# Performance work log

Measured on AMD Instinct MI355X. Metric: run time of the kernel, lower is better.

The kernel has to match this reference:

```python
import jax, jax.numpy as jnp
import numpy as np

HEADS = 8
LATENT_LEN = 64
SEQ_LEN = 8192
DIM = 512
DIM_HEAD = DIM // HEADS
LN_EPS = 1e-5


def setup_inputs() -> dict:
    key = jax.random.key(0)
    k1, k2, k3 = jax.random.split(key, 3)
    b, n = 16, SEQ_LEN + LATENT_LEN
    x = jax.random.normal(k1, (b, n, DIM), dtype=jnp.float32)
    # torch nn.Linear weights are [out_features, in_features]
    wq = jax.random.normal(k2, (DIM, DIM), dtype=jnp.float32) * (DIM ** -0.5)
    wkv = jax.random.normal(k3, (DIM, DIM), dtype=jnp.float32) * (DIM ** -0.5)
    ln_g = jnp.ones((DIM_HEAD,), dtype=jnp.float32)
    ln_b = jnp.zeros((DIM_HEAD,), dtype=jnp.float32)
    return {"x": x, "wq": wq, "wkv": wkv, "ln_g": ln_g, "ln_b": ln_b}


def _rotate_half(t):
    # lucidrains-style rotate_half: split last dim in two halves, (-x2, x1)
    d2 = t.shape[-1] // 2
    t1, t2 = t[..., :d2], t[..., d2:]
    return jnp.concatenate([-t2, t1], axis=-1)


def _rotary_emb(n, d, dtype):
    inv_freq = 1.0 / (10000.0 ** (jnp.arange(0, d, 2, dtype=jnp.float32) / d))
    freqs = jnp.arange(n, dtype=jnp.float32)[:, None] * inv_freq[None, :]  # [n, d/2]
    emb = jnp.concatenate([freqs, freqs], axis=-1)  # [n, d]
    return jnp.cos(emb).astype(dtype), jnp.sin(emb).astype(dtype)


def reference(x, wq, wkv, ln_g, ln_b):
    b, n, dim = x.shape
    h, d = HEADS, DIM_HEAD
    context_len = n - LATENT_LEN
    scale = d ** -0.5

    q = x @ wq.T   # [b, n, dim]
    kv = x @ wkv.T # [b, n, dim]
    # rearrange 'b n (h d) -> (b h) n d'
    to_bh = lambda t: t.reshape(b, n, h, d).transpose(0, 2, 1, 3).reshape(b * h, n, d)
    q, kv = to_bh(q), to_bh(kv)

    cos, sin = _rotary_emb(n, d, x.dtype)  # [n, d] broadcast over (b h)
    rope = lambda t: t * cos + _rotate_half(t) * sin
    q, kv = rope(q), rope(kv)

    q = q * scale
    q_latent = q[:, context_len:, :]  # [(b h), latent, d]

    # LayerNorm over head dim applied to V (kv)
    mu = jnp.mean(kv, axis=-1, keepdims=True)
    var = jnp.mean(jnp.square(kv - mu), axis=-1, keepdims=True)
    lkv = (kv - mu) * jax.lax.rsqrt(var + LN_EPS) * ln_g + ln_b

    sim = jnp.einsum('bid,bjd->bij', q_latent, kv)  # [(b h), latent, n]
    attn = jax.nn.softmax(sim, axis=-1)
    out = jnp.einsum('bij,bjd->bid', attn, lkv)     # [(b h), latent, d]

    # rearrange '(b h) n d -> b n (h d)'
    out = out.reshape(b, h, LATENT_LEN, d).transpose(0, 2, 1, 3).reshape(b, LATENT_LEN, dim)
    return out
```

## Files before the change

### kernel.cpp

```cpp
#include <hip/hip_runtime.h>
#include <hip/hip_bf16.h>
#include <math.h>

#define SEQ_LEN 8192
#define LAT 64
#define NPOS 8256
#define NBATCH 16
#define NHEADS 8
#define DH 64
#define DIM 512
#define NBH 128
#define NROWS 132096
#define NCHUNK 8
#define NTILES 129
#define TPC 17

typedef unsigned short u16;
typedef unsigned int   u32;
using short8 = __attribute__((ext_vector_type(8))) short;
using f32x4  = __attribute__((ext_vector_type(4))) float;

static __device__ __forceinline__ float bf2f(u16 u) {
  union { u32 i; float f; } v; v.i = ((u32)u) << 16; return v.f;
}
static __device__ __forceinline__ u16 f2bf(float f) {
  union { float f; u32 i; } v; v.f = f;
  u32 x = v.i;
  return (u16)((x + 0x7fffu + ((x >> 16) & 1u)) >> 16);
}
static __device__ __forceinline__ void gload_lds16(const void* g, void* l) {
  __builtin_amdgcn_global_load_lds(
      (const __attribute__((address_space(1))) unsigned int*)g,
      (__attribute__((address_space(3))) unsigned int*)l, 16, 0, 0);
}

__global__ void k_rtable(float* __restrict__ ctab, float* __restrict__ stab) {
  int idx = blockIdx.x * 256 + threadIdx.x;
  int pos = idx >> 5, i = idx & 31;
  float inv = (float)(1.0 / pow(10000.0, (double)(2 * i) / 64.0));
  float ang = (float)pos * inv;
  ctab[idx] = cosf(ang);
  stab[idx] = sinf(ang);
}

__global__ __launch_bounds__(256) void k_wcast(const float* __restrict__ wkv, u16* __restrict__ wbf) {
  size_t i = (size_t)blockIdx.x * 256 + threadIdx.x;
  const float4* src = (const float4*)wkv;
  float4 a = src[2 * i], b = src[2 * i + 1];
  uint4 o;
  o.x = (u32)f2bf(a.x) | ((u32)f2bf(a.y) << 16);
  o.y = (u32)f2bf(a.z) | ((u32)f2bf(a.w) << 16);
  o.z = (u32)f2bf(b.x) | ((u32)f2bf(b.y) << 16);
  o.w = (u32)f2bf(b.z) | ((u32)f2bf(b.w) << 16);
  ((uint4*)wbf)[i] = o;
}

__global__ __launch_bounds__(256) void k_qproj(
    const float* __restrict__ x, const float* __restrict__ wq,
    const float* __restrict__ ctab, const float* __restrict__ stab,
    u16* __restrict__ qws) {
  __shared__ __align__(16) float xs[8 * 512];
  int t = threadIdx.x;
  int lr0 = blockIdx.x * 8;
  int batch = lr0 >> 6;
  int lat0 = lr0 & 63;
  for (int u = 0; u < 4; ++u) {
    int e = u * 256 + t;
    int row = e >> 7, c4 = e & 127;
    size_t m = (size_t)batch * NPOS + SEQ_LEN + lat0 + row;
    ((float4*)xs)[e] = ((const float4*)(x + m * DIM))[c4];
  }
  __syncthreads();
  float acc0[8], acc1[8];
#pragma unroll
  for (int r = 0; r < 8; ++r) { acc0[r] = 0.f; acc1[r] = 0.f; }
  const float4* w0 = (const float4*)(wq + (size_t)t * DIM);
  const float4* w1 = (const float4*)(wq + (size_t)(t + 256) * DIM);
  for (int kk = 0; kk < 128; ++kk) {
    float4 a = w0[kk], b = w1[kk];
#pragma unroll
    for (int r = 0; r < 8; ++r) {
      float4 xv = ((const float4*)xs)[r * 128 + kk];
      acc0[r] = fmaf(a.x, xv.x, fmaf(a.y, xv.y, fmaf(a.z, xv.z, fmaf(a.w, xv.w, acc0[r]))));
      acc1[r] = fmaf(b.x, xv.x, fmaf(b.y, xv.y, fmaf(b.z, xv.z, fmaf(b.w, xv.w, acc1[r]))));
    }
  }
  __syncthreads();
#pragma unroll
  for (int r = 0; r < 8; ++r) { xs[r * 512 + t] = acc0[r]; xs[r * 512 + t + 256] = acc1[r]; }
  __syncthreads();
  int rh = t >> 2, sub = t & 3;
  int row = rh >> 3, head = rh & 7;
  int lat = lat0 + row, pos = SEQ_LEN + lat;
  int bh = batch * 8 + head;
  u16* qd = qws + ((size_t)bh * LAT + lat) * DH;
#pragma unroll
  for (int u = 0; u < 8; ++u) {
    int i = sub * 8 + u;
    float v1 = xs[row * 512 + head * 64 + i];
    float v2 = xs[row * 512 + head * 64 + i + 32];
    float cc = ctab[pos * 32 + i], ss = stab[pos * 32 + i];
    qd[i]      = f2bf((v1 * cc - v2 * ss) * 0.125f);
    qd[i + 32] = f2bf((v2 * cc + v1 * ss) * 0.125f);
  }
}

__global__ __launch_bounds__(256, 2) void k_kvgemm(
    const float* __restrict__ x, const u16* __restrict__ wbf,
    const float* __restrict__ ctab, const float* __restrict__ stab,
    u16* __restrict__ kvws, float2* __restrict__ stats) {
  __shared__ __align__(16) char smem[65536];
  float* Cs = (float*)smem;
  int t = threadIdx.x;
  int lane = t & 63, w = t >> 6;
  int wr = w >> 1, wc = w & 1;
  int c = lane & 15, g = lane >> 4;
  int s = (blockIdx.x & 7) * 516 + (blockIdx.x >> 3);
  int n0 = (s & 3) * 128;
  size_t m0 = (size_t)(s >> 2) * 128;

  f32x4 acc[4][4];
#pragma unroll
  for (int mt = 0; mt < 4; ++mt)
#pragma unroll
    for (int nt = 0; nt < 4; ++nt) acc[mt][nt] = (f32x4){0.f, 0.f, 0.f, 0.f};

  int ar = t >> 3, ac8 = t & 7;
  const float* axbase = x + (m0 + ar) * DIM + ac8 * 8;
  int aswz = (ac8 * 16) ^ ((ar & 7) << 4);
  int tcs = ((t & 7) ^ (ar & 7)) << 4;
  const char* bgsrc = (const char*)(wbf + (size_t)(n0 + ar) * DIM) + tcs;

  float4 a0[4], a1[4];
  auto issueA = [&](int kt) {
#pragma unroll
    for (int u = 0; u < 4; ++u) {
      const float* p = axbase + (size_t)u * 32 * DIM + kt * 64;
      a0[u] = *(const float4*)p;
      a1[u] = *(const float4*)(p + 4);
    }
  };
  auto issueB = [&](int kt, char* bbuf) {
    const char* bg = bgsrc + kt * 128;
    char* bl = bbuf + t * 16;
#pragma unroll
    for (int u = 0; u < 4; ++u) gload_lds16(bg + (size_t)u * 32 * 1024, bl + u * 4096);
  };
  auto writeA = [&](char* abuf) {
#pragma unroll
    for (int u = 0; u < 4; ++u) {
      short8 o;
      o[0] = (short)f2bf(a0[u].x); o[1] = (short)f2bf(a0[u].y);
      o[2] = (short)f2bf(a0[u].z); o[3] = (short)f2bf(a0[u].w);
      o[4] = (short)f2bf(a1[u].x); o[5] = (short)f2bf(a1[u].y);
      o[6] = (short)f2bf(a1[u].z); o[7] = (short)f2bf(a1[u].w);
      *(short8*)(abuf + (u * 32 + ar) * 128 + aswz) = o;
    }
  };

  issueA(0);
  issueB(0, smem + 32768);
  writeA(smem);
  __syncthreads();

#pragma unroll
  for (int kt = 0; kt < 8; ++kt) {
    char* Acur = smem + (kt & 1) * 16384;
    char* Bcur = smem + 32768 + (kt & 1) * 16384;
    char* Anxt = smem + ((kt & 1) ^ 1) * 16384;
    char* Bnxt = smem + 32768 + ((kt & 1) ^ 1) * 16384;
    if (kt < 7) { issueA(kt + 1); issueB(kt + 1, Bnxt); }
#pragma unroll
    for (int ks = 0; ks < 2; ++ks) {
      short8 am[4], bn[4];
#pragma unroll
      for (int mt = 0; mt < 4; ++mt) {
        int row = wr * 64 + mt * 16 + c;
        am[mt] = *(const short8*)(Acur + row * 128 + ((ks * 64 + g * 16) ^ ((row & 7) << 4)));
      }
#pragma unroll
      for (int nt = 0; nt < 4; ++nt) {
        int row = wc * 64 + nt * 16 + c;
        bn[nt] = *(const short8*)(Bcur + row * 128 + ((ks * 64 + g * 16) ^ ((row & 7) << 4)));
      }
#pragma unroll
      for (int mt = 0; mt < 4; ++mt)
#pragma unroll
        for (int nt = 0; nt < 4; ++nt)
          acc[mt][nt] = __builtin_amdgcn_mfma_f32_16x16x32_bf16(am[mt], bn[nt], acc[mt][nt], 0, 0, 0);
    }
    if (kt < 7) writeA(Anxt);
    __syncthreads();
  }

  for (int p = 0; p < 2; ++p) {
    __syncthreads();
    if (wr == p) {
#pragma unroll
      for (int mt = 0; mt < 4; ++mt)
#pragma unroll
        for (int nt = 0; nt < 4; ++nt)
#pragma unroll
          for (int r = 0; r < 4; ++r)
            Cs[(mt * 16 + 4 * g + r) * 132 + wc * 64 + nt * 16 + c] = acc[mt][nt][r];
    }
    __syncthreads();
    if (t < 128) {
      int r_ = t & 63, hh = t >> 6;
      float v[64];
      const float4* crow = (const float4*)(Cs + r_ * 132 + hh * 64);
#pragma unroll
      for (int q = 0; q < 16; ++q) {
        float4 f = crow[q];
        v[4 * q] = f.x; v[4 * q + 1] = f.y; v[4 * q + 2] = f.z; v[4 * q + 3] = f.w;
      }
      int mi = (int)(m0 + p * 64 + r_);
      int b = mi / NPOS, pos = mi % NPOS;
      const float* ct = ctab + pos * 32;
      const float* st = stab + pos * 32;
#pragma unroll
      for (int i = 0; i < 32; ++i) {
        float cc = ct[i], ss = st[i];
        float v1 = v[i], v2 = v[i + 32];
        v[i]      = v1 * cc - v2 * ss;
        v[i + 32] = v2 * cc + v1 * ss;
      }
      float sum = 0.f;
#pragma unroll
      for (int e = 0; e < 64; ++e) sum += v[e];
      float mu = sum * 0.015625f;
      float sq = 0.f;
#pragma unroll
      for (int e = 0; e < 64; ++e) { float d = v[e] - mu; sq = fmaf(d, d, sq); }
      float rstd = rsqrtf(sq * 0.015625f + 1e-5f);
      int head = (n0 >> 6) + hh;
      int bh = b * 8 + head;
      u32 pk[32];
#pragma unroll
      for (int e = 0; e < 32; ++e) pk[e] = (u32)f2bf(v[2 * e]) | ((u32)f2bf(v[2 * e + 1]) << 16);
      uint4* dst = (uint4*)(kvws + ((size_t)bh * NPOS + pos) * DH);
#pragma unroll
      for (int u = 0; u < 8; ++u) dst[u] = make_uint4(pk[4 * u], pk[4 * u + 1], pk[4 * u + 2], pk[4 * u + 3]);
      stats[(size_t)bh * NPOS + pos] = make_float2(mu, rstd);
    }
  }
}

__global__ __launch_bounds__(256) void k_attn(
    const u16* __restrict__ qws, const u16* __restrict__ kvws,
    const float2* __restrict__ stats,
    float* __restrict__ pout, float* __restrict__ pml) {
  __shared__ __align__(16) u16 LT[64 * 64];
  __shared__ __align__(16) u16 Pl[4][16 * 64];
  int t = threadIdx.x;
  int lane = t & 63, w = t >> 6;
  int c = lane & 15, g = lane >> 4;
  int bh = blockIdx.y, chunk = blockIdx.x;
  int tt0 = chunk * TPC;
  int tt1 = tt0 + TPC; if (tt1 > NTILES) tt1 = NTILES;
  short8 qa[2];
  {
    const u16* qrow = qws + ((size_t)bh * LAT + w * 16 + c) * DH;
    qa[0] = *(const short8*)(qrow + 8 * g);
    qa[1] = *(const short8*)(qrow + 32 + 8 * g);
  }
  f32x4 oacc[4];
#pragma unroll
  for (int nt = 0; nt < 4; ++nt) oacc[nt] = (f32x4){0.f, 0.f, 0.f, 0.f};
  float m_run[4], l_run[4], q2_run[4];
#pragma unroll
  for (int r = 0; r < 4; ++r) { m_run[r] = -INFINITY; l_run[r] = 0.f; q2_run[r] = 0.f; }
  int sj = t & 63, sw = t >> 6;
  for (int tt = tt0; tt < tt1; ++tt) {
    int j0 = tt * 64;
    __syncthreads();
    {
      const u16* src = kvws + ((size_t)bh * NPOS + j0 + sj) * DH + 16 * sw;
      short8 v0 = *(const short8*)src;
      short8 v1 = *(const short8*)(src + 8);
      char* ltb = (char*)LT;
#pragma unroll
      for (int e = 0; e < 16; ++e) {
        int dd = 16 * sw + e;
        u16 uv = (u16)((e < 8) ? v0[e] : v1[e - 8]);
        *(u16*)(ltb + dd * 128 + ((2 * sj) ^ ((dd & 7) << 4))) = uv;
      }
    }
    __syncthreads();
    f32x4 sacc[4];
#pragma unroll
    for (int jn = 0; jn < 4; ++jn) sacc[jn] = (f32x4){0.f, 0.f, 0.f, 0.f};
    const u16* kb = kvws + ((size_t)bh * NPOS + j0) * DH;
#pragma unroll
    for (int ks = 0; ks < 2; ++ks)
#pragma unroll
      for (int jn = 0; jn < 4; ++jn) {
        short8 kf = *(const short8*)(kb + (size_t)(jn * 16 + c) * DH + ks * 32 + 8 * g);
        sacc[jn] = __builtin_amdgcn_mfma_f32_16x16x32_bf16(qa[ks], kf, sacc[jn], 0, 0, 0);
      }
    float rsd[4], musig[4];
#pragma unroll
    for (int jn = 0; jn < 4; ++jn) {
      float2 sv = stats[(size_t)bh * NPOS + j0 + jn * 16 + c];
      rsd[jn] = sv.y; musig[jn] = sv.x * sv.y;
    }
    char* pb = (char*)Pl[w];
#pragma unroll
    for (int r = 0; r < 4; ++r) {
      float mt0 = fmaxf(fmaxf(sacc[0][r], sacc[1][r]), fmaxf(sacc[2][r], sacc[3][r]));
      mt0 = fmaxf(mt0, __shfl_xor(mt0, 1));
      mt0 = fmaxf(mt0, __shfl_xor(mt0, 2));
      mt0 = fmaxf(mt0, __shfl_xor(mt0, 4));
      mt0 = fmaxf(mt0, __shfl_xor(mt0, 8));
      float mnew = fmaxf(m_run[r], mt0);
      float corr = __expf(m_run[r] - mnew);
      m_run[r] = mnew;
      float ts = 0.f, tq = 0.f;
#pragma unroll
      for (int jn = 0; jn < 4; ++jn) {
        float p = __expf(sacc[jn][r] - mnew);
        ts += p;
        tq = fmaf(p, musig[jn], tq);
        sacc[jn][r] = p * rsd[jn];
      }
      ts += __shfl_xor(ts, 1); ts += __shfl_xor(ts, 2);
      ts += __shfl_xor(ts, 4); ts += __shfl_xor(ts, 8);
      tq += __shfl_xor(tq, 1); tq += __shfl_xor(tq, 2);
      tq += __shfl_xor(tq, 4); tq += __shfl_xor(tq, 8);
      l_run[r]  = l_run[r]  * corr + ts;
      q2_run[r] = q2_run[r] * corr + tq;
#pragma unroll
      for (int nt = 0; nt < 4; ++nt) oacc[nt][r] *= corr;
      int i = 4 * g + r;
      int isw = (i & 7) << 4;
#pragma unroll
      for (int jn = 0; jn < 4; ++jn) {
        int j = jn * 16 + c;
        *(u16*)(pb + i * 128 + ((2 * j) ^ isw)) = f2bf(sacc[jn][r]);
      }
    }
#pragma unroll
    for (int ks = 0; ks < 2; ++ks) {
      short8 pa = *(const short8*)(pb + c * 128 + ((ks * 64 + 16 * g) ^ ((c & 7) << 4)));
#pragma unroll
      for (int nt = 0; nt < 4; ++nt) {
        int dd = nt * 16 + c;
        short8 lv = *(const short8*)((char*)LT + dd * 128 + ((ks * 64 + 16 * g) ^ ((dd & 7) << 4)));
        oacc[nt] = __builtin_amdgcn_mfma_f32_16x16x32_bf16(pa, lv, oacc[nt], 0, 0, 0);
      }
    }
  }
  size_t ob = (size_t)bh * NCHUNK + chunk;
#pragma unroll
  for (int nt = 0; nt < 4; ++nt)
#pragma unroll
    for (int r = 0; r < 4; ++r) {
      int i = w * 16 + 4 * g + r;
      pout[(ob * 64 + i) * 64 + nt * 16 + c] = oacc[nt][r];
    }
  if (c == 0) {
#pragma unroll
    for (int r = 0; r < 4; ++r) {
      int i = w * 16 + 4 * g + r;
      pml[(ob * 3 + 0) * 64 + i] = m_run[r];
      pml[(ob * 3 + 1) * 64 + i] = l_run[r];
      pml[(ob * 3 + 2) * 64 + i] = q2_run[r];
    }
  }
}

__global__ __launch_bounds__(256) void k_combine(
    const float* __restrict__ pout, const float* __restrict__ pml,
    const float* __restrict__ lng, const float* __restrict__ lnb,
    float* __restrict__ out) {
  int bh = blockIdx.x, t = threadIdx.x;
  int i = t >> 2, dq = t & 3;
  float mv[NCHUNK], lv[NCHUNK], qv[NCHUNK];
#pragma unroll
  for (int cc = 0; cc < NCHUNK; ++cc) {
    size_t ob = (size_t)bh * NCHUNK + cc;
    mv[cc] = pml[(ob * 3 + 0) * 64 + i];
    lv[cc] = pml[(ob * 3 + 1) * 64 + i];
    qv[cc] = pml[(ob * 3 + 2) * 64 + i];
  }
  float M = -INFINITY;
#pragma unroll
  for (int cc = 0; cc < NCHUNK; ++cc) M = fmaxf(M, mv[cc]);
  float L = 0.f, Q2 = 0.f, wcf[NCHUNK];
#pragma unroll
  for (int cc = 0; cc < NCHUNK; ++cc) {
    wcf[cc] = __expf(mv[cc] - M);
    L = fmaf(wcf[cc], lv[cc], L);
    Q2 = fmaf(wcf[cc], qv[cc], Q2);
  }
  float invL = 1.0f / L;
#pragma unroll
  for (int e = 0; e < 16; ++e) {
    int dd = dq * 16 + e;
    float O = 0.f;
#pragma unroll
    for (int cc = 0; cc < NCHUNK; ++cc)
      O = fmaf(wcf[cc], pout[(((size_t)bh * NCHUNK + cc) * 64 + i) * 64 + dd], O);
    float val = (lng[dd] * (O - Q2) + lnb[dd] * L) * invL;
    out[((size_t)(bh >> 3) * LAT + i) * DIM + (bh & 7) * DH + dd] = val;
  }
}

extern "C" void kernel_launch(void* const* d_in, const int* in_sizes, int n_in,
                              void* d_out, int out_size, void* d_ws, size_t ws_size,
                              hipStream_t stream) {
  const float* x   = (const float*)d_in[0];
  const float* wq  = (const float*)d_in[1];
  const float* wkv = (const float*)d_in[2];
  const float* lng = (const float*)d_in[3];
  const float* lnb = (const float*)d_in[4];
  float* out = (float*)d_out;
  char* ws = (char*)d_ws;
  size_t off = 0;
  auto alloc = [&](size_t bytes) { char* p = ws + off; off += (bytes + 255) & ~(size_t)255; return p; };
  float*  ctab  = (float*)alloc((size_t)NPOS * 32 * 4);
  float*  stab  = (float*)alloc((size_t)NPOS * 32 * 4);
  u16*    qws   = (u16*)alloc((size_t)NBH * LAT * DH * 2);
  u16*    kvws  = (u16*)alloc((size_t)NBH * NPOS * DH * 2);
  float2* stats = (float2*)alloc((size_t)NBH * NPOS * 8);
  float*  pout  = (float*)alloc((size_t)NBH * NCHUNK * 64 * 64 * 4);
  float*  pml   = (float*)alloc((size_t)NBH * NCHUNK * 3 * 64 * 4);
  u16*    wbf   = (u16*)alloc((size_t)DIM * DIM * 2);
  (void)in_sizes; (void)n_in; (void)out_size; (void)ws_size;

  hipLaunchKernelGGL(k_rtable, dim3(NPOS * 32 / 256), dim3(256), 0, stream, ctab, stab);
  hipLaunchKernelGGL(k_wcast, dim3(DIM * DIM / 8 / 256), dim3(256), 0, stream, wkv, wbf);
  hipLaunchKernelGGL(k_qproj, dim3(128), dim3(256), 0, stream, x, wq, ctab, stab, qws);
  hipLaunchKernelGGL(k_kvgemm, dim3(4128), dim3(256), 0, stream, x, wbf, ctab, stab, kvws, stats);
  hipLaunchKernelGGL(k_attn, dim3(NCHUNK, NBH), dim3(256), 0, stream, qws, kvws, stats, pout, pml);
  hipLaunchKernelGGL(k_combine, dim3(NBH), dim3(256), 0, stream, pout, pml, lng, lnb, out);
}
```

Measured before the change: 412.1 us.

## Rewrite KV GEMM as LDS-free per-wave tiles with register epilogue

Result: slower. 617.9 us (+49.9%).

```diff
diff --git a/kernel.cpp b/kernel.cpp
--- a/kernel.cpp
+++ b/kernel.cpp
@@ -11,9 +11,9 @@
 #define DIM 512
 #define NBH 128
 #define NROWS 132096
-#define NCHUNK 8
+#define NCHUNK 4
 #define NTILES 129
-#define TPC 17
+#define TPC 33
 
 typedef unsigned short u16;
 typedef unsigned int   u32;
@@ -27,11 +27,6 @@
   union { float f; u32 i; } v; v.f = f;
   u32 x = v.i;
   return (u16)((x + 0x7fffu + ((x >> 16) & 1u)) >> 16);
-}
-static __device__ __forceinline__ void gload_lds16(const void* g, void* l) {
-  __builtin_amdgcn_global_load_lds(
-      (const __attribute__((address_space(1))) unsigned int*)g,
-      (__attribute__((address_space(3))) unsigned int*)l, 16, 0, 0);
 }
 
 __global__ void k_rtable(float* __restrict__ ctab, float* __restrict__ stab) {
@@ -105,19 +100,19 @@
   }
 }
 
-__global__ __launch_bounds__(256, 2) void k_kvgemm(
+__global__ __launch_bounds__(256, 3) void k_kvgemm(
     const float* __restrict__ x, const u16* __restrict__ wbf,
     const float* __restrict__ ctab, const float* __restrict__ stab,
     u16* __restrict__ kvws, float2* __restrict__ stats) {
-  __shared__ __align__(16) char smem[65536];
-  float* Cs = (float*)smem;
-  int t = threadIdx.x;
-  int lane = t & 63, w = t >> 6;
-  int wr = w >> 1, wc = w & 1;
-  int c = lane & 15, g = lane >> 4;
-  int s = (blockIdx.x & 7) * 516 + (blockIdx.x >> 3);
-  int n0 = (s & 3) * 128;
-  size_t m0 = (size_t)(s >> 2) * 128;
+  const int t = threadIdx.x;
+  const int lane = t & 63, w = t >> 6;
+  const int c = lane & 15, g = lane >> 4;
+  const int s = (blockIdx.x & 7) * 516 + (blockIdx.x >> 3);
+  const int mtile = s >> 1, nhalf = s & 1;
+  const size_t m0 = (size_t)mtile * 64;
+  const int n0 = nhalf * 256 + w * 64;
+  const int b = mtile / 129;
+  const int pos0 = (mtile % 129) * 64;
 
   f32x4 acc[4][4];
 #pragma unroll
@@ -125,123 +120,71 @@
 #pragma unroll
     for (int nt = 0; nt < 4; ++nt) acc[mt][nt] = (f32x4){0.f, 0.f, 0.f, 0.f};
 
-  int ar = t >> 3, ac8 = t & 7;
-  const float* axbase = x + (m0 + ar) * DIM + ac8 * 8;
-  int aswz = (ac8 * 16) ^ ((ar & 7) << 4);
-  int tcs = ((t & 7) ^ (ar & 7)) << 4;
-  const char* bgsrc = (const char*)(wbf + (size_t)(n0 + ar) * DIM) + tcs;
-
-  float4 a0[4], a1[4];
-  auto issueA = [&](int kt) {
-#pragma unroll
-    for (int u = 0; u < 4; ++u) {
-      const float* p = axbase + (size_t)u * 32 * DIM + kt * 64;
-      a0[u] = *(const float4*)p;
-      a1[u] = *(const float4*)(p + 4);
-    }
-  };
-  auto issueB = [&](int kt, char* bbuf) {
-    const char* bg = bgsrc + kt * 128;
-    char* bl = bbuf + t * 16;
-#pragma unroll
-    for (int u = 0; u < 4; ++u) gload_lds16(bg + (size_t)u * 32 * 1024, bl + u * 4096);
-  };
-  auto writeA = [&](char* abuf) {
-#pragma unroll
-    for (int u = 0; u < 4; ++u) {
+  const float* a0p = x + (m0 + c) * DIM + g * 8;
+  const u16*   b0p = wbf + (size_t)(n0 + c) * DIM + g * 8;
+
+#pragma unroll 4
+  for (int ks = 0; ks < 16; ++ks) {
+    const int ko = ks * 32;
+    short8 bn[4];
+#pragma unroll
+    for (int nt = 0; nt < 4; ++nt)
+      bn[nt] = *(const short8*)(b0p + (size_t)nt * 16 * DIM + ko);
+    short8 am[4];
+#pragma unroll
+    for (int mt = 0; mt < 4; ++mt) {
+      const float* ap = a0p + (size_t)mt * 16 * DIM + ko;
+      float4 lo = *(const float4*)ap;
+      float4 hi = *(const float4*)(ap + 4);
       short8 o;
-      o[0] = (short)f2bf(a0[u].x); o[1] = (short)f2bf(a0[u].y);
-      o[2] = (short)f2bf(a0[u].z); o[3] = (short)f2bf(a0[u].w);
-      o[4] = (short)f2bf(a1[u].x); o[5] = (short)f2bf(a1[u].y);
-      o[6] = (short)f2bf(a1[u].z); o[7] = (short)f2bf(a1[u].w);
-      *(short8*)(abuf + (u * 32 + ar) * 128 + aswz) = o;
-    }
-  };
-
-  issueA(0);
-  issueB(0, smem + 32768);
-  writeA(smem);
-  __syncthreads();
-
-#pragma unroll
-  for (int kt = 0; kt < 8; ++kt) {
-    char* Acur = smem + (kt & 1) * 16384;
-    char* Bcur = smem + 32768 + (kt & 1) * 16384;
-    char* Anxt = smem + ((kt & 1) ^ 1) * 16384;
-    char* Bnxt = smem + 32768 + ((kt & 1) ^ 1) * 16384;
-    if (kt < 7) { issueA(kt + 1); issueB(kt + 1, Bnxt); }
-#pragma unroll
-    for (int ks = 0; ks < 2; ++ks) {
-      short8 am[4], bn[4];
-#pragma unroll
-      for (int mt = 0; mt < 4; ++mt) {
-        int row = wr * 64 + mt * 16 + c;
-        am[mt] = *(const short8*)(Acur + row * 128 + ((ks * 64 + g * 16) ^ ((row & 7) << 4)));
-      }
-#pragma unroll
-      for (int nt = 0; nt < 4; ++nt) {
-        int row = wc * 64 + nt * 16 + c;
-        bn[nt] = *(const short8*)(Bcur + row * 128 + ((ks * 64 + g * 16) ^ ((row & 7) << 4)));
-      }
-#pragma unroll
-      for (int mt = 0; mt < 4; ++mt)
-#pragma unroll
-        for (int nt = 0; nt < 4; ++nt)
-          acc[mt][nt] = __builtin_amdgcn_mfma_f32_16x16x32_bf16(am[mt], bn[nt], acc[mt][nt], 0, 0, 0);
-    }
-    if (kt < 7) writeA(Anxt);
-    __syncthreads();
-  }
-
-  for (int p = 0; p < 2; ++p) {
-    __syncthreads();
-    if (wr == p) {
-#pragma unroll
-      for (int mt = 0; mt < 4; ++mt)
-#pragma unroll
-        for (int nt = 0; nt < 4; ++nt)
-#pragma unroll
-          for (int r = 0; r < 4; ++r)
-            Cs[(mt * 16 + 4 * g + r) * 132 + wc * 64 + nt * 16 + c] = acc[mt][nt][r];
-    }
-    __syncthreads();
-    if (t < 128) {
-      int r_ = t & 63, hh = t >> 6;
-      float v[64];
-      const float4* crow = (const float4*)(Cs + r_ * 132 + hh * 64);
-#pragma unroll
-      for (int q = 0; q < 16; ++q) {
-        float4 f = crow[q];
-        v[4 * q] = f.x; v[4 * q + 1] = f.y; v[4 * q + 2] = f.z; v[4 * q + 3] = f.w;
-      }
-      int mi = (int)(m0 + p * 64 + r_);
-      int b = mi / NPOS, pos = mi % NPOS;
-      const float* ct = ctab + pos * 32;
-      const float* st = stab + pos * 32;
-#pragma unroll
-      for (int i = 0; i < 32; ++i) {
-        float cc = ct[i], ss = st[i];
-        float v1 = v[i], v2 = v[i + 32];
-        v[i]      = v1 * cc - v2 * ss;
-        v[i + 32] = v2 * cc + v1 * ss;
-      }
-      float sum = 0.f;
-#pragma unroll
-      for (int e = 0; e < 64; ++e) sum += v[e];
+      o[0] = (short)__bfloat16_as_ushort(__float2bfloat16(lo.x));
+      o[1] = (short)__bfloat16_as_ushort(__float2bfloat16(lo.y));
+      o[2] = (short)__bfloat16_as_ushort(__float2bfloat16(lo.z));
+      o[3] = (short)__bfloat16_as_ushort(__float2bfloat16(lo.w));
+      o[4] = (short)__bfloat16_as_ushort(__float2bfloat16(hi.x));
+      o[5] = (short)__bfloat16_as_ushort(__float2bfloat16(hi.y));
+      o[6] = (short)__bfloat16_as_ushort(__float2bfloat16(hi.z));
+      o[7] = (short)__bfloat16_as_ushort(__float2bfloat16(hi.w));
+      am[mt] = o;
+    }
+#pragma unroll
+    for (int mt = 0; mt < 4; ++mt)
+#pragma unroll
+      for (int nt = 0; nt < 4; ++nt)
+        acc[mt][nt] = __builtin_amdgcn_mfma_f32_16x16x32_bf16(am[mt], bn[nt], acc[mt][nt], 0, 0, 0);
+  }
+
+  const int head = n0 >> 6;
+  const int bh = b * 8 + head;
+#pragma unroll
+  for (int mt = 0; mt < 4; ++mt) {
+#pragma unroll
+    for (int r = 0; r < 4; ++r) {
+      const int row = mt * 16 + 4 * g + r;
+      const int pos = pos0 + row;
+      float cc0 = ctab[pos * 32 + c],      ss0 = stab[pos * 32 + c];
+      float cc1 = ctab[pos * 32 + 16 + c], ss1 = stab[pos * 32 + 16 + c];
+      float v1a = acc[mt][0][r], v2a = acc[mt][2][r];
+      float v1b = acc[mt][1][r], v2b = acc[mt][3][r];
+      float o0 = v1a * cc0 - v2a * ss0;
+      float o2 = v2a * cc0 + v1a * ss0;
+      float o1 = v1b * cc1 - v2b * ss1;
+      float o3 = v2b * cc1 + v1b * ss1;
+      float sum = (o0 + o1) + (o2 + o3);
+      sum += __shfl_xor(sum, 1); sum += __shfl_xor(sum, 2);
+      sum += __shfl_xor(sum, 4); sum += __shfl_xor(sum, 8);
       float mu = sum * 0.015625f;
-      float sq = 0.f;
-#pragma unroll
-      for (int e = 0; e < 64; ++e) { float d = v[e] - mu; sq = fmaf(d, d, sq); }
+      float d0 = o0 - mu, d1 = o1 - mu, d2 = o2 - mu, d3 = o3 - mu;
+      float sq = fmaf(d0, d0, fmaf(d1, d1, fmaf(d2, d2, d3 * d3)));
+      sq += __shfl_xor(sq, 1); sq += __shfl_xor(sq, 2);
+      sq += __shfl_xor(sq, 4); sq += __shfl_xor(sq, 8);
       float rstd = rsqrtf(sq * 0.015625f + 1e-5f);
-      int head = (n0 >> 6) + hh;
-      int bh = b * 8 + head;
-      u32 pk[32];
-#pragma unroll
-      for (int e = 0; e < 32; ++e) pk[e] = (u32)f2bf(v[2 * e]) | ((u32)f2bf(v[2 * e + 1]) << 16);
-      uint4* dst = (uint4*)(kvws + ((size_t)bh * NPOS + pos) * DH);
-#pragma unroll
-      for (int u = 0; u < 8; ++u) dst[u] = make_uint4(pk[4 * u], pk[4 * u + 1], pk[4 * u + 2], pk[4 * u + 3]);
-      stats[(size_t)bh * NPOS + pos] = make_float2(mu, rstd);
+      u16* kvp = kvws + ((size_t)bh * NPOS + pos) * DH;
+      kvp[c]      = f2bf(o0);
+      kvp[16 + c] = f2bf(o1);
+      kvp[32 + c] = f2bf(o2);
+      kvp[48 + c] = f2bf(o3);
+      if (c == 0) stats[(size_t)bh * NPOS + pos] = make_float2(mu, rstd);
     }
   }
 }
```
